# Performance work log

Hardware: AMD Instinct MI355X
Metric: run time of the kernel (lower is better)

The kernel has to match this reference:

```python
import jax, jax.numpy as jnp
import numpy as np

K = 7          # neighborhood kernel size (7x7)
NH = 8         # num heads


def _nbr_idx(n):
    # NATTEN-style clamped windows: window start = clip(i - K//2, 0, n-K)
    pos = jnp.arange(n)
    start = jnp.clip(pos - K // 2, 0, n - K)          # (n,)
    idx = start[:, None] + jnp.arange(K)[None, :]     # (n, K) absolute key positions
    rel = idx - pos[:, None] + (K - 1)                # (n, K) in [0, 2K-2] for rpb lookup
    return idx, rel


def _forward(x, w_qkv, b_qkv, rpb, w_proj, b_proj, w_fc1, b_fc1, w_fc2, b_fc2):
    B, C, H, W = x.shape
    hd = C // NH
    scale = hd ** -0.5

    # ---- neighborhood attention (norm0 = Identity) ----
    xp = jnp.transpose(x, (0, 2, 3, 1))                           # (B,H,W,C)
    qkv = xp @ w_qkv + b_qkv                                      # (B,H,W,3C)
    qkv = qkv.reshape(B, H, W, 3, NH, hd)
    q = qkv[:, :, :, 0] * scale                                   # (B,H,W,nh,hd)
    k = qkv[:, :, :, 1]
    v = qkv[:, :, :, 2]

    idx_h, rel_h = _nbr_idx(H)                                    # (H,K)
    idx_w, rel_w = _nbr_idx(W)                                    # (W,K)

    # gather 7x7 neighborhoods: (B,H,K,W,K,nh,hd)
    k_nbr = k[:, idx_h][:, :, :, idx_w]
    v_nbr = v[:, idx_h][:, :, :, idx_w]

    # attention logits: (B,H,W,nh,K,K)
    attn = jnp.einsum('bxynd,bxiyjnd->bxynij', q, k_nbr)
    # relative positional bias: rpb (nh, 2K-1, 2K-1) -> (nh,H,K,W,K)
    bias = rpb[:, rel_h][:, :, :, rel_w]                          # (nh,H,K,W,K)
    attn = attn + jnp.transpose(bias, (1, 3, 0, 2, 4))[None]      # (B,H,W,nh,K,K)

    attn = jax.nn.softmax(attn.reshape(B, H, W, NH, K * K), axis=-1)
    attn = attn.reshape(B, H, W, NH, K, K)

    out = jnp.einsum('bxynij,bxiyjnd->bxynd', attn, v_nbr)        # (B,H,W,nh,hd)
    out = out.reshape(B, H, W, C) @ w_proj + b_proj               # (B,H,W,C)
    x1 = jnp.transpose(out, (0, 3, 1, 2)) + x                     # residual skip0

    # ---- MLP (1x1-conv style, channels-first; norm1 = Identity) ----
    h = jnp.einsum('bchw,cf->bfhw', x1, w_fc1) + b_fc1[None, :, None, None]
    h = jax.nn.gelu(h, approximate=False)                         # torch nn.GELU (erf)
    y = jnp.einsum('bfhw,fc->bchw', h, w_fc2) + b_fc2[None, :, None, None]
    return y + x1                                                 # residual skip1


def setup_inputs() -> dict:
    key = jax.random.key(0)
    B, C, H, W = 1, 256, 64, 128
    hid = int(C * 2.0)
    ks = jax.random.split(key, 8)
    s = 0.02
    return {
        'x': jax.random.normal(ks[0], (B, C, H, W), jnp.float32),
        'w_qkv': jax.random.normal(ks[1], (C, 3 * C), jnp.float32) * s,
        'b_qkv': jnp.zeros((3 * C,), jnp.float32),
        'rpb': jax.random.normal(ks[2], (NH, 2 * K - 1, 2 * K - 1), jnp.float32) * s,
        'w_proj': jax.random.normal(ks[3], (C, C), jnp.float32) * s,
        'b_proj': jnp.zeros((C,), jnp.float32),
        'w_fc1': jax.random.normal(ks[4], (C, hid), jnp.float32) * s,
        'b_fc1': jnp.zeros((hid,), jnp.float32),
        'w_fc2': jax.random.normal(ks[5], (hid, C), jnp.float32) * s,
        'b_fc2': jnp.zeros((C,), jnp.float32),
    }


def reference(x, w_qkv, b_qkv, rpb, w_proj, b_proj, w_fc1, b_fc1, w_fc2, b_fc2):
    return _forward(x, w_qkv, b_qkv, rpb, w_proj, b_proj, w_fc1, b_fc1, w_fc2, b_fc2)
```

## Files before the change

### kernel.cpp

```cpp
#include <hip/hip_runtime.h>

typedef unsigned short ushort;
typedef short bf16x8 __attribute__((ext_vector_type(8)));
typedef float f32x4 __attribute__((ext_vector_type(4)));

static __device__ __forceinline__ ushort f2b(float f) {
  unsigned u = __builtin_bit_cast(unsigned, f);
  u = (u + 0x7fffu + ((u >> 16) & 1u)) >> 16;
  return (ushort)u;
}

__global__ __launch_bounds__(256) void prep_kernel(
    const float* __restrict__ x,
    const float* __restrict__ w_qkv, const float* __restrict__ w_proj,
    const float* __restrict__ w_fc1, const float* __restrict__ w_fc2,
    ushort* __restrict__ xb, ushort* __restrict__ wqkvT,
    ushort* __restrict__ wprojT, ushort* __restrict__ wfc1T,
    ushort* __restrict__ wfc2T)
{
  int i = blockIdx.x * 256 + threadIdx.x;
  if (i < 2097152) {
    int c = i & 255, m = i >> 8;
    xb[i] = f2b(x[(size_t)c * 8192 + m]);
    return;
  }
  i -= 2097152;
  if (i < 196608) {
    int k = i & 255, n = i >> 8;
    wqkvT[i] = f2b(w_qkv[(size_t)k * 768 + n]);
    return;
  }
  i -= 196608;
  if (i < 65536) {
    int k = i & 255, n = i >> 8;
    wprojT[i] = f2b(w_proj[(size_t)k * 256 + n]);
    return;
  }
  i -= 65536;
  if (i < 131072) {
    int k = i & 255, n = i >> 8;
    wfc1T[i] = f2b(w_fc1[(size_t)k * 512 + n]);
    return;
  }
  i -= 131072;
  if (i < 131072) {
    int k = i & 511, n = i >> 9;
    wfc2T[i] = f2b(w_fc2[(size_t)k * 256 + n]);
  }
}

template<int EPI>
__global__ __launch_bounds__(256) void gemm_mfma(
    const ushort* __restrict__ A, const ushort* __restrict__ Bt,
    const float* __restrict__ bias, const float* __restrict__ R,
    void* __restrict__ C0, void* __restrict__ C1,
    int M, int N, int K)
{
  __shared__ __attribute__((aligned(16))) ushort As[64 * 40];
  __shared__ __attribute__((aligned(16))) ushort Bs[64 * 40];

  const int bm = blockIdx.y * 64;
  const int bn = blockIdx.x * 64;
  const int t  = threadIdx.x;
  const int w    = t >> 6;
  const int lane = t & 63;
  const int wm = (w & 1) * 32;
  const int wn = (w >> 1) * 32;
  const int lm = lane & 15;
  const int kq = lane >> 4;

  const int sm = t >> 2;
  const int sk = (t & 3) * 8;

  f32x4 acc[2][2] = {};

  for (int k0 = 0; k0 < K; k0 += 32) {
    *(uint4*)(&As[sm * 40 + sk]) = *(const uint4*)(A  + (size_t)(bm + sm) * K + k0 + sk);
    *(uint4*)(&Bs[sm * 40 + sk]) = *(const uint4*)(Bt + (size_t)(bn + sm) * K + k0 + sk);
    __syncthreads();

    bf16x8 a0 = *(const bf16x8*)(&As[(wm + lm)      * 40 + kq * 8]);
    bf16x8 a1 = *(const bf16x8*)(&As[(wm + 16 + lm) * 40 + kq * 8]);
    bf16x8 b0 = *(const bf16x8*)(&Bs[(wn + lm)      * 40 + kq * 8]);
    bf16x8 b1 = *(const bf16x8*)(&Bs[(wn + 16 + lm) * 40 + kq * 8]);
    acc[0][0] = __builtin_amdgcn_mfma_f32_16x16x32_bf16(a0, b0, acc[0][0], 0, 0, 0);
    acc[0][1] = __builtin_amdgcn_mfma_f32_16x16x32_bf16(a0, b1, acc[0][1], 0, 0, 0);
    acc[1][0] = __builtin_amdgcn_mfma_f32_16x16x32_bf16(a1, b0, acc[1][0], 0, 0, 0);
    acc[1][1] = __builtin_amdgcn_mfma_f32_16x16x32_bf16(a1, b1, acc[1][1], 0, 0, 0);
    __syncthreads();
  }

  #pragma unroll
  for (int ti = 0; ti < 2; ti++) {
    #pragma unroll
    for (int tj = 0; tj < 2; tj++) {
      const int n  = bn + wn + tj * 16 + lm;
      const int m0 = bm + wm + ti * 16 + kq * 4;
      if (EPI == 3) {
        float4 v;
        float* vp = &v.x;
        #pragma unroll
        for (int r = 0; r < 4; r++)
          vp[r] = acc[ti][tj][r] + bias[n] + R[(size_t)(m0 + r) * 256 + n];
        *(float4*)((float*)C0 + (size_t)n * M + m0) = v;
      } else if (EPI == 0) {
        if (n < 512) {
          #pragma unroll
          for (int r = 0; r < 4; r++)
            ((ushort*)C0)[(size_t)(m0 + r) * N + n] = f2b(acc[ti][tj][r] + bias[n]);
        } else {
          ushort4 st;
          st.x = f2b(acc[ti][tj][0] + bias[n]);
          st.y = f2b(acc[ti][tj][1] + bias[n]);
          st.z = f2b(acc[ti][tj][2] + bias[n]);
          st.w = f2b(acc[ti][tj][3] + bias[n]);
          *(ushort4*)((ushort*)C1 + (size_t)(n - 512) * 8192 + m0) = st;
        }
      } else {
        #pragma unroll
        for (int r = 0; r < 4; r++) {
          const int m = m0 + r;
          float v = acc[ti][tj][r] + bias[n];
          if (EPI == 1) {
            v += R[(size_t)n * M + m];
            ((float*)C0)[(size_t)m * 256 + n] = v;
            ((ushort*)C1)[(size_t)m * 256 + n] = f2b(v);
          } else {
            v = 0.5f * v * (1.0f + erff(v * 0.70710678118f));
            ((ushort*)C0)[(size_t)m * N + n] = f2b(v);
          }
        }
      }
    }
  }
}

__global__ __launch_bounds__(256) void natt_mfma(
    const ushort* __restrict__ qkv, const ushort* __restrict__ vT,
    const float* __restrict__ rpb, ushort* __restrict__ att)
{
  __shared__ __attribute__((aligned(16))) ushort Plds[4][7][16][40];
  __shared__ float Rlds[4][176];

  const int w    = threadIdx.x >> 6;
  const int lane = threadIdx.x & 63;
  const int l  = lane & 15;
  const int q  = lane >> 4;
  const int tile = blockIdx.x;
  const int n    = blockIdx.y * 4 + w;
  const int ph  = tile >> 3;
  const int pw0 = (tile & 7) << 4;
  const int p0  = ph * 128 + pw0;

  int sh = ph - 3;  sh = sh < 0 ? 0 : (sh > 57 ? 57 : sh);
  int sb = pw0 - 3; sb = sb < 0 ? 0 : sb;
  const int sba = sb & ~7;

  const float L2E = 1.44269504f;
  for (int idx = lane; idx < 169; idx += 64)
    Rlds[w][idx] = rpb[n * 169 + idx] * L2E;

  bf16x8 qf = *(const bf16x8*)(qkv + (size_t)(p0 + l) * 768 + n * 32 + q * 8);

  f32x4 s[7][2] = {};
  #pragma unroll
  for (int i = 0; i < 7; i++) {
    const int rowp = (sh + i) * 128;
    #pragma unroll
    for (int h = 0; h < 2; h++) {
      int jc = sba + h * 16 + l;
      jc = jc > 127 ? 127 : jc;
      bf16x8 kf = *(const bf16x8*)(qkv + (size_t)(rowp + jc) * 768 + 256 + n * 32 + q * 8);
      s[i][h] = __builtin_amdgcn_mfma_f32_16x16x32_bf16(qf, kf, s[i][h], 0, 0, 0);
    }
  }
  __syncthreads();

  const float KSC = 0.17677669529663689f * 1.44269504f;
  const int relh0 = sh - ph + 6;
  float rsum[4] = {0.f, 0.f, 0.f, 0.f};
  #pragma unroll
  for (int r = 0; r < 4; r++) {
    const int pw = pw0 + q * 4 + r;
    int sw = pw - 3; sw = sw < 0 ? 0 : (sw > 121 ? 121 : sw);
    #pragma unroll
    for (int h = 0; h < 2; h++) {
      const int jc = sba + h * 16 + l;
      const bool valid = (unsigned)(jc - sw) <= 6u;
      int relw = jc - pw + 6;
      relw = relw < 0 ? 0 : (relw > 12 ? 12 : relw);
      #pragma unroll
      for (int i = 0; i < 7; i++) {
        float b = Rlds[w][(relh0 + i) * 13 + relw];
        float v = s[i][h][r] * KSC + b;
        v = valid ? v : -1e30f;
        float e = exp2f(v);
        s[i][h][r] = e;
        rsum[r] += e;
      }
    }
  }
  #pragma unroll
  for (int r = 0; r < 4; r++) {
    rsum[r] += __shfl_xor(rsum[r], 1);
    rsum[r] += __shfl_xor(rsum[r], 2);
    rsum[r] += __shfl_xor(rsum[r], 4);
    rsum[r] += __shfl_xor(rsum[r], 8);
  }

  #pragma unroll
  for (int i = 0; i < 7; i++)
    #pragma unroll
    for (int h = 0; h < 2; h++)
      #pragma unroll
      for (int r = 0; r < 4; r++)
        Plds[w][i][q * 4 + r][h * 16 + l] = f2b(s[i][h][r]);
  __syncthreads();

  f32x4 o[2] = {};
  #pragma unroll
  for (int i = 0; i < 7; i++) {
    bf16x8 pf = *(const bf16x8*)(&Plds[w][i][l][q * 8]);
    const int rowp = (sh + i) * 128;
    #pragma unroll
    for (int dh = 0; dh < 2; dh++) {
      bf16x8 vf = *(const bf16x8*)(vT + (size_t)(n * 32 + dh * 16 + l) * 8192
                                      + rowp + sba + q * 8);
      o[dh] = __builtin_amdgcn_mfma_f32_16x16x32_bf16(pf, vf, o[dh], 0, 0, 0);
    }
  }

  #pragma unroll
  for (int r = 0; r < 4; r++) {
    const float inv = 1.0f / rsum[r];
    #pragma unroll
    for (int dh = 0; dh < 2; dh++)
      att[(size_t)(p0 + q * 4 + r) * 256 + n * 32 + dh * 16 + l] = f2b(o[dh][r] * inv);
  }
}

extern "C" void kernel_launch(void* const* d_in, const int* in_sizes, int n_in,
                              void* d_out, int out_size, void* d_ws, size_t ws_size,
                              hipStream_t stream)
{
  const float* x      = (const float*)d_in[0];
  const float* w_qkv  = (const float*)d_in[1];
  const float* b_qkv  = (const float*)d_in[2];
  const float* rpb    = (const float*)d_in[3];
  const float* w_proj = (const float*)d_in[4];
  const float* b_proj = (const float*)d_in[5];
  const float* w_fc1  = (const float*)d_in[6];
  const float* b_fc1  = (const float*)d_in[7];
  const float* w_fc2  = (const float*)d_in[8];
  const float* b_fc2  = (const float*)d_in[9];
  float* out = (float*)d_out;

  const int M = 8192;
  char* ws = (char*)d_ws;
  ushort* xb     = (ushort*)(ws);
  ushort* qkv    = (ushort*)(ws + 4194304);
  float*  x1f    = (float*)(ws + 16777216);
  ushort* x1b    = (ushort*)(ws + 25165824);
  ushort* wqkvT  = (ushort*)(ws + 29360128);
  ushort* wprojT = (ushort*)(ws + 29753344);
  ushort* wfc1T  = (ushort*)(ws + 29884416);
  ushort* wfc2T  = (ushort*)(ws + 30146560);
  ushort* vT     = (ushort*)(ws + 30408704);
  ushort* att = xb;
  ushort* h   = qkv;

  dim3 blk(256);

  prep_kernel<<<dim3(10240), blk, 0, stream>>>(
      x, w_qkv, w_proj, w_fc1, w_fc2, xb, wqkvT, wprojT, wfc1T, wfc2T);

  gemm_mfma<0><<<dim3(768 / 64, M / 64), blk, 0, stream>>>(
      xb, wqkvT, b_qkv, nullptr, qkv, vT, M, 768, 256);

  natt_mfma<<<dim3(512, 2), blk, 0, stream>>>(qkv, vT, rpb, att);

  gemm_mfma<1><<<dim3(256 / 64, M / 64), blk, 0, stream>>>(
      att, wprojT, b_proj, x, x1f, x1b, M, 256, 256);

  gemm_mfma<2><<<dim3(512 / 64, M / 64), blk, 0, stream>>>(
      x1b, wfc1T, b_fc1, nullptr, h, nullptr, M, 512, 256);

  gemm_mfma<3><<<dim3(256 / 64, M / 64), blk, 0, stream>>>(
      h, wfc2T, b_fc2, x1f, out, nullptr, M, 256, 512);
}
```

Before: 154.2 us.

## Enlarge GEMM tiles and load operands directly into LDS

The MFMA GEMM tile grows from 64x64 to 128xTN, with TN templated as 128 or 64 per call. Each wave now computes a 4xFJ grid of 16x16 fragments, which raises operand reuse per LDS load. Global-to-shared copies now use global_load_lds, which writes straight to LDS without passing through registers. The padded LDS layout (stride 40) is replaced by an unpadded stride of 32, which may cause bank conflicts, and the larger tiles produce fewer blocks, which lowers occupancy on small grids.

```diff
diff --git a/kernel.cpp b/kernel.cpp
--- a/kernel.cpp
+++ b/kernel.cpp
@@ -49,78 +49,100 @@
   }
 }
 
-template<int EPI>
+template<int EPI, int TN>
 __global__ __launch_bounds__(256) void gemm_mfma(
     const ushort* __restrict__ A, const ushort* __restrict__ Bt,
     const float* __restrict__ bias, const float* __restrict__ R,
     void* __restrict__ C0, void* __restrict__ C1,
     int M, int N, int K)
 {
-  __shared__ __attribute__((aligned(16))) ushort As[64 * 40];
-  __shared__ __attribute__((aligned(16))) ushort Bs[64 * 40];
-
-  const int bm = blockIdx.y * 64;
-  const int bn = blockIdx.x * 64;
+  constexpr int FJ = TN / 32;
+  __shared__ __attribute__((aligned(16))) ushort As[128 * 32];
+  __shared__ __attribute__((aligned(16))) ushort Bs[TN * 32];
+
+  const int bm = blockIdx.y * 128;
+  const int bn = blockIdx.x * TN;
   const int t  = threadIdx.x;
   const int w    = t >> 6;
   const int lane = t & 63;
-  const int wm = (w & 1) * 32;
-  const int wn = (w >> 1) * 32;
   const int lm = lane & 15;
   const int kq = lane >> 4;
-
-  const int sm = t >> 2;
-  const int sk = (t & 3) * 8;
-
-  f32x4 acc[2][2] = {};
+  const int wm = (w & 1) * 64;
+  const int wn = (w >> 1) * (TN / 2);
+
+  const int lrow = lane >> 2;
+  const int lcol = (lane & 3) * 8;
+
+  f32x4 acc[4][FJ] = {};
 
   for (int k0 = 0; k0 < K; k0 += 32) {
-    *(uint4*)(&As[sm * 40 + sk]) = *(const uint4*)(A  + (size_t)(bm + sm) * K + k0 + sk);
-    *(uint4*)(&Bs[sm * 40 + sk]) = *(const uint4*)(Bt + (size_t)(bn + sm) * K + k0 + sk);
+    #pragma unroll
+    for (int s = 0; s < 2; s++) {
+      const int issue = w + s * 4;
+      const ushort* gp = A + (size_t)(bm + issue * 16 + lrow) * K + k0 + lcol;
+      __builtin_amdgcn_global_load_lds(
+          (const __attribute__((address_space(1))) unsigned*)gp,
+          (__attribute__((address_space(3))) unsigned*)(As + issue * 512),
+          16, 0, 0);
+    }
+    #pragma unroll
+    for (int s = 0; s < TN / 64; s++) {
+      const int issue = w + s * 4;
+      const ushort* gp = Bt + (size_t)(bn + issue * 16 + lrow) * K + k0 + lcol;
+      __builtin_amdgcn_global_load_lds(
+          (const __attribute__((address_space(1))) unsigned*)gp,
+          (__attribute__((address_space(3))) unsigned*)(Bs + issue * 512),
+          16, 0, 0);
+    }
     __syncthreads();
 
-    bf16x8 a0 = *(const bf16x8*)(&As[(wm + lm)      * 40 + kq * 8]);
-    bf16x8 a1 = *(const bf16x8*)(&As[(wm + 16 + lm) * 40 + kq * 8]);
-    bf16x8 b0 = *(const bf16x8*)(&Bs[(wn + lm)      * 40 + kq * 8]);
-    bf16x8 b1 = *(const bf16x8*)(&Bs[(wn + 16 + lm) * 40 + kq * 8]);
-    acc[0][0] = __builtin_amdgcn_mfma_f32_16x16x32_bf16(a0, b0, acc[0][0], 0, 0, 0);
-    acc[0][1] = __builtin_amdgcn_mfma_f32_16x16x32_bf16(a0, b1, acc[0][1], 0, 0, 0);
-    acc[1][0] = __builtin_amdgcn_mfma_f32_16x16x32_bf16(a1, b0, acc[1][0], 0, 0, 0);
-    acc[1][1] = __builtin_amdgcn_mfma_f32_16x16x32_bf16(a1, b1, acc[1][1], 0, 0, 0);
+    bf16x8 af[4], bfr[FJ];
+    #pragma unroll
+    for (int fi = 0; fi < 4; fi++)
+      af[fi] = *(const bf16x8*)(As + (wm + fi * 16 + lm) * 32 + kq * 8);
+    #pragma unroll
+    for (int fj = 0; fj < FJ; fj++)
+      bfr[fj] = *(const bf16x8*)(Bs + (wn + fj * 16 + lm) * 32 + kq * 8);
+    #pragma unroll
+    for (int fi = 0; fi < 4; fi++)
+      #pragma unroll
+      for (int fj = 0; fj < FJ; fj++)
+        acc[fi][fj] = __builtin_amdgcn_mfma_f32_16x16x32_bf16(
+            af[fi], bfr[fj], acc[fi][fj], 0, 0, 0);
     __syncthreads();
   }
 
   #pragma unroll
-  for (int ti = 0; ti < 2; ti++) {
-    #pragma unroll
-    for (int tj = 0; tj < 2; tj++) {
-      const int n  = bn + wn + tj * 16 + lm;
-      const int m0 = bm + wm + ti * 16 + kq * 4;
+  for (int fi = 0; fi < 4; fi++) {
+    #pragma unroll
+    for (int fj = 0; fj < FJ; fj++) {
+      const int n  = bn + wn + fj * 16 + lm;
+      const int m0 = bm + wm + fi * 16 + kq * 4;
       if (EPI == 3) {
         float4 v;
         float* vp = &v.x;
         #pragma unroll
         for (int r = 0; r < 4; r++)
-          vp[r] = acc[ti][tj][r] + bias[n] + R[(size_t)(m0 + r) * 256 + n];
+          vp[r] = acc[fi][fj][r] + bias[n] + R[(size_t)(m0 + r) * 256 + n];
         *(float4*)((float*)C0 + (size_t)n * M + m0) = v;
       } else if (EPI == 0) {
         if (n < 512) {
           #pragma unroll
           for (int r = 0; r < 4; r++)
-            ((ushort*)C0)[(size_t)(m0 + r) * N + n] = f2b(acc[ti][tj][r] + bias[n]);
+            ((ushort*)C0)[(size_t)(m0 + r) * N + n] = f2b(acc[fi][fj][r] + bias[n]);
         } else {
           ushort4 st;
-          st.x = f2b(acc[ti][tj][0] + bias[n]);
-          st.y = f2b(acc[ti][tj][1] + bias[n]);
-          st.z = f2b(acc[ti][tj][2] + bias[n]);
-          st.w = f2b(acc[ti][tj][3] + bias[n]);
+          st.x = f2b(acc[fi][fj][0] + bias[n]);
+          st.y = f2b(acc[fi][fj][1] + bias[n]);
+          st.z = f2b(acc[fi][fj][2] + bias[n]);
+          st.w = f2b(acc[fi][fj][3] + bias[n]);
           *(ushort4*)((ushort*)C1 + (size_t)(n - 512) * 8192 + m0) = st;
         }
       } else {
         #pragma unroll
         for (int r = 0; r < 4; r++) {
           const int m = m0 + r;
-          float v = acc[ti][tj][r] + bias[n];
+          float v = acc[fi][fj][r] + bias[n];
           if (EPI == 1) {
             v += R[(size_t)n * M + m];
             ((float*)C0)[(size_t)m * 256 + n] = v;
@@ -274,17 +296,17 @@
   prep_kernel<<<dim3(10240), blk, 0, stream>>>(
       x, w_qkv, w_proj, w_fc1, w_fc2, xb, wqkvT, wprojT, wfc1T, wfc2T);
 
-  gemm_mfma<0><<<dim3(768 / 64, M / 64), blk, 0, stream>>>(
+  gemm_mfma<0, 128><<<dim3(768 / 128, M / 128), blk, 0, stream>>>(
       xb, wqkvT, b_qkv, nullptr, qkv, vT, M, 768, 256);
 
   natt_mfma<<<dim3(512, 2), blk, 0, stream>>>(qkv, vT, rpb, att);
 
-  gemm_mfma<1><<<dim3(256 / 64, M / 64), blk, 0, stream>>>(
+  gemm_mfma<1, 64><<<dim3(256 / 64, M / 128), blk, 0, stream>>>(
       att, wprojT, b_proj, x, x1f, x1b, M, 256, 256);
 
-  gemm_mfma<2><<<dim3(512 / 64, M / 64), blk, 0, stream>>>(
+  gemm_mfma<2, 128><<<dim3(512 / 128, M / 128), blk, 0, stream>>>(
       x1b, wfc1T, b_fc1, nullptr, h, nullptr, M, 512, 256);
 
-  gemm_mfma<3><<<dim3(256 / 64, M / 64), blk, 0, stream>>>(
+  gemm_mfma<3, 64><<<dim3(256 / 64, M / 128), blk, 0, stream>>>(
       h, wfc2T, b_fc2, x1f, out, nullptr, M, 256, 512);
 }
```

Result: slower. 163.5 us (+6.0%).
